# Optimization experiments

Measured on AMD Instinct MI355X. Metric: run time of the kernel, lower is better.

Reference implementation:

```python
import jax, jax.numpy as jnp
import numpy as np
import math

D_MODEL, N_HEADS, D_HEAD, D_MLP = 768, 12, 64, 3072
EPS = 1e-5
IGNORE = -100000.0


def _ln(x, w, b):
    mu = jnp.mean(x, axis=-1, keepdims=True)
    xc = x - mu
    scale = jnp.sqrt(jnp.mean(xc * xc, axis=-1, keepdims=True) + EPS)
    return (xc / scale) * w + b


def _gelu_new(x):
    # GPT-2 'new' gelu
    return 0.5 * x * (1.0 + jnp.tanh(jnp.sqrt(2.0 / jnp.pi) * (x + 0.044715 * x ** 3)))


def setup_inputs() -> dict:
    key = jax.random.key(0)
    ks = jax.random.split(key, 12)
    std = 0.02
    inp = {
        "resid_pre": jax.random.normal(ks[0], (8, 1024, D_MODEL), jnp.float32),
        "W_Q": jax.random.normal(ks[1], (N_HEADS, D_MODEL, D_HEAD), jnp.float32) * std,
        "b_Q": jnp.zeros((N_HEADS, D_HEAD), jnp.float32),
        "W_K": jax.random.normal(ks[2], (N_HEADS, D_MODEL, D_HEAD), jnp.float32) * std,
        "b_K": jnp.zeros((N_HEADS, D_HEAD), jnp.float32),
        "W_V": jax.random.normal(ks[3], (N_HEADS, D_MODEL, D_HEAD), jnp.float32) * std,
        "b_V": jnp.zeros((N_HEADS, D_HEAD), jnp.float32),
        "W_O": jax.random.normal(ks[4], (N_HEADS, D_HEAD, D_MODEL), jnp.float32) * std,
        "b_O": jnp.zeros((D_MODEL,), jnp.float32),
        "ln1_w": jnp.ones((D_MODEL,), jnp.float32),
        "ln1_b": jnp.zeros((D_MODEL,), jnp.float32),
        "ln2_w": jnp.ones((D_MODEL,), jnp.float32),
        "ln2_b": jnp.zeros((D_MODEL,), jnp.float32),
        "W_in": jax.random.normal(ks[5], (D_MODEL, D_MLP), jnp.float32) * std,
        "b_in": jnp.zeros((D_MLP,), jnp.float32),
        "W_out": jax.random.normal(ks[6], (D_MLP, D_MODEL), jnp.float32) * std,
        "b_out": jnp.zeros((D_MODEL,), jnp.float32),
    }
    return inp


def reference(resid_pre, W_Q, b_Q, W_K, b_K, W_V, b_V, W_O, b_O,
              ln1_w, ln1_b, ln2_w, ln2_b, W_in, b_in, W_out, b_out):
    # ---- ln1 + attention ----
    n = _ln(resid_pre, ln1_w, ln1_b)  # [b, s, d]; broadcast over heads in einsums
    q = jnp.einsum('bsd,hde->bshe', n, W_Q) + b_Q
    k = jnp.einsum('bsd,hde->bshe', n, W_K) + b_K
    v = jnp.einsum('bsd,hde->bshe', n, W_V) + b_V
    scores = jnp.einsum('bqhe,bkhe->bhqk', q, k) / math.sqrt(D_HEAD)
    S = scores.shape[-1]
    causal = jnp.triu(jnp.ones((S, S), dtype=bool), k=1)
    scores = jnp.where(causal, IGNORE, scores)
    pattern = jax.nn.softmax(scores, axis=-1)
    z = jnp.einsum('bhqk,bkhe->bqhe', pattern, v)
    # per-head output with b_O / n_heads each (as in source), then summed over heads
    attn_per_head = jnp.einsum('bqhe,hed->bqhd', z, W_O) + b_O / N_HEADS
    attn_out = attn_per_head.sum(axis=2)  # [b, s, d]
    resid_mid = resid_pre + attn_out
    # ---- ln2 + mlp ----
    n2 = _ln(resid_mid, ln2_w, ln2_b)
    pre = jnp.einsum('bsd,dm->bsm', n2, W_in) + b_in
    post = _gelu_new(pre)
    mlp_out = jnp.einsum('bsm,md->bsd', post, W_out) + b_out
    return resid_mid + mlp_out
```

## Files before the change

kernel.cpp:

```cpp
#include <hip/hip_runtime.h>
#include <hip/hip_bf16.h>

typedef unsigned short u16;
typedef float f32x4 __attribute__((ext_vector_type(4)));
typedef __bf16 bf16x8 __attribute__((ext_vector_type(8)));
typedef unsigned short u16x8 __attribute__((ext_vector_type(8)));
typedef unsigned short u16x4 __attribute__((ext_vector_type(4)));

__device__ __forceinline__ float b2f(u16 u) {
    unsigned v = ((unsigned)u) << 16;
    return __builtin_bit_cast(float, v);
}
__device__ __forceinline__ u16 f2b(float f) {
    unsigned u = __builtin_bit_cast(unsigned, f);
    u += 0x7fffu + ((u >> 16) & 1u);
    return (u16)(u >> 16);
}
__device__ __forceinline__ bf16x8 ldfrag(const u16* p) {
    return __builtin_bit_cast(bf16x8, *(const u16x8*)p);
}
__device__ __forceinline__ f32x4 mfma16(bf16x8 a, bf16x8 b, f32x4 c) {
    return __builtin_amdgcn_mfma_f32_16x16x32_bf16(a, b, c, 0, 0, 0);
}
__device__ __forceinline__ void gload_lds16(const u16* g, u16* l) {
    __builtin_amdgcn_global_load_lds(
        (const __attribute__((address_space(1))) unsigned int*)(g),
        (__attribute__((address_space(3))) unsigned int*)(l), 16, 0, 0);
}

#define T_TOK 8192
#define DM 768
#define NH 12
#define DH 64
#define DMLP 3072
#define SEQ 1024
#define QKV_LD 2304
#define QK_LD 1536

#define OFF_WQKV ((size_t)0)
#define OFF_WO   (OFF_WQKV + (size_t)2304*768)
#define OFF_WIN  (OFF_WO   + (size_t)768*768)
#define OFF_WOUT (OFF_WIN  + (size_t)768*3072)
#define OFF_BQKV (OFF_WOUT + (size_t)3072*768)
#define P0       (OFF_BQKV + (size_t)4608)

#define SZ_N    ((size_t)T_TOK*DM)
#define SZ_QKV  ((size_t)T_TOK*QKV_LD)
#define A_NBUF   (P0)
#define A_QKV    (P0 + SZ_N)
#define A_Z      (P0 + SZ_N + SZ_QKV)
#define A_N2     (P0)
#define A_POST   (P0 + SZ_N)
#define PATHA_BYTES (((size_t)(P0 + SZ_N + SZ_QKV + SZ_N)) * 2)
#define B_Z      (P0)
#define B_QKVB   (P0 + SZ_N)
#define B_NBUF   (B_QKVB + (size_t)SEQ*QKV_LD)
#define B_N2     (P0)
#define B_POSTC  (P0 + SZ_N)

#define TT_QKV  432
#define TT_WO   (TT_QKV + 144)
#define TT_WIN  (TT_WO + 576)
#define TT_WOUT (TT_WIN + 576)

__global__ __launch_bounds__(256) void prep_kernel(
    const float* __restrict__ WQ, const float* __restrict__ WK, const float* __restrict__ WV,
    const float* __restrict__ WO, const float* __restrict__ Win, const float* __restrict__ Wout,
    const float* __restrict__ bQ, const float* __restrict__ bK, const float* __restrict__ bV,
    u16* __restrict__ Wqkv_t, u16* __restrict__ Wo_t, u16* __restrict__ Win_t,
    u16* __restrict__ Wout_t, float* __restrict__ bias_qkv)
{
    const int bid = blockIdx.x;
    const int tid = threadIdx.x;
    if (bid == TT_WOUT) {
        for (int j = tid; j < 2304; j += 256)
            bias_qkv[j] = (j < 768) ? bQ[j] : ((j < 1536) ? bK[j - 768] : bV[j - 1536]);
        return;
    }
    __shared__ u16 tile[64][72];

    const float* sp; u16* dp;
    int sldc, dldc;
    if (bid < TT_QKV) {
        int wh = bid / 12, td = bid % 12;
        int which = wh / 12, h = wh % 12;
        const float* W = (which == 0) ? WQ : ((which == 1) ? WK : WV);
        sp = W + (size_t)h * 49152 + (size_t)(td * 64) * 64;   sldc = 64;
        dp = Wqkv_t + (size_t)(which * 768 + h * 64) * 768 + td * 64; dldc = 768;
    } else if (bid < TT_WO) {
        int t2 = bid - TT_QKV, ti = t2 / 12, tj = t2 % 12;
        sp = WO + (size_t)(ti * 64) * 768 + tj * 64;           sldc = 768;
        dp = Wo_t + (size_t)(tj * 64) * 768 + ti * 64;         dldc = 768;
    } else if (bid < TT_WIN) {
        int t3 = bid - TT_WO, ti = t3 / 48, tj = t3 % 48;
        sp = Win + (size_t)(ti * 64) * 3072 + tj * 64;         sldc = 3072;
        dp = Win_t + (size_t)(tj * 64) * 768 + ti * 64;        dldc = 768;
    } else {
        int t4 = bid - TT_WIN, ti = t4 / 12, tj = t4 % 12;
        sp = Wout + (size_t)(ti * 64) * 768 + tj * 64;         sldc = 768;
        dp = Wout_t + (size_t)(tj * 64) * 3072 + ti * 64;      dldc = 3072;
    }

    {
        int r = tid >> 2, cseg = (tid & 3) * 16;
        const float* src = sp + (size_t)r * sldc + cseg;
#pragma unroll
        for (int j = 0; j < 16; j++)
            tile[cseg + j][r] = f2b(src[j]);
    }
    __syncthreads();
    {
        int r2 = tid >> 2, c2seg = (tid & 3) * 16;
        u16* dst = dp + (size_t)r2 * dldc + c2seg;
        *(u16x8*)dst       = *(const u16x8*)&tile[r2][c2seg];
        *(u16x8*)(dst + 8) = *(const u16x8*)&tile[r2][c2seg + 8];
    }
}

__global__ __launch_bounds__(256) void ln_kernel(
    const float* __restrict__ x, const float* __restrict__ w,
    const float* __restrict__ bb, u16* __restrict__ out)
{
    __shared__ float red[4];
    size_t base = (size_t)blockIdx.x * DM;
    int tid = threadIdx.x;
    float v0 = x[base + tid], v1 = x[base + tid + 256], v2 = x[base + tid + 512];
    float s = v0 + v1 + v2;
#pragma unroll
    for (int off = 32; off > 0; off >>= 1) s += __shfl_xor(s, off);
    if ((tid & 63) == 0) red[tid >> 6] = s;
    __syncthreads();
    float mu = (red[0] + red[1] + red[2] + red[3]) * (1.0f / 768.0f);
    v0 -= mu; v1 -= mu; v2 -= mu;
    float q = v0 * v0 + v1 * v1 + v2 * v2;
    __syncthreads();
#pragma unroll
    for (int off = 32; off > 0; off >>= 1) q += __shfl_xor(q, off);
    if ((tid & 63) == 0) red[tid >> 6] = q;
    __syncthreads();
    float var = (red[0] + red[1] + red[2] + red[3]) * (1.0f / 768.0f);
    float sc = rsqrtf(var + 1e-5f);
    out[base + tid]       = f2b(v0 * sc * w[tid]       + bb[tid]);
    out[base + tid + 256] = f2b(v1 * sc * w[tid + 256] + bb[tid + 256]);
    out[base + tid + 512] = f2b(v2 * sc * w[tid + 512] + bb[tid + 512]);
}

template <int EPI, int TM>
__global__ __launch_bounds__(256) void gemm_bt_kernel(
    const u16* __restrict__ A, const u16* __restrict__ BT,
    const float* __restrict__ bias, const float* __restrict__ aux,
    void* __restrict__ outp, int N, int K)
{
    __shared__ __align__(16) u16 As[3][TM * 32];
    __shared__ __align__(16) u16 Bs[3][128 * 32];
    const int tid = threadIdx.x;
    const int w = tid >> 6, l = tid & 63;
    const int lr = l & 15, lq = l >> 4;
    const int bm = blockIdx.x * TM, bn = blockIdx.y * 128;
    constexpr int MT = TM / 32;
    constexpr bool TR = (EPI != 4);
    const int wm = (w >> 1) * (TM / 2), wn = (w & 1) * 64;

    f32x4 acc[MT][4];
#pragma unroll
    for (int i = 0; i < MT; i++)
#pragma unroll
        for (int j = 0; j < 4; j++) acc[i][j] = f32x4{0.f, 0.f, 0.f, 0.f};

    const int srow_a = (TM == 128) ? (w * 32 + (l >> 2)) : (w * 16 + (l >> 2));
    const int srow_b = w * 32 + (l >> 2);
    const int scol = (l & 3) * 8;
    const u16* Ab = A  + (size_t)(bm + srow_a) * K + scol;
    const u16* Bb = BT + (size_t)(bn + srow_b) * K + scol;
    const int asd = (TM == 128) ? w * 1024 : w * 512;
    const int bsd = w * 1024;

    const int kiter = K >> 5;

#define STAGE_T(kk, s)                                                      \
    {   const int k0_ = (kk) * 32;                                          \
        gload_lds16(Ab + k0_, &As[s][asd]);                                 \
        if constexpr (TM == 128) gload_lds16(Ab + 16 * K + k0_, &As[s][asd + 512]); \
        gload_lds16(Bb + k0_,          &Bs[s][bsd]);                        \
        gload_lds16(Bb + 16 * K + k0_, &Bs[s][bsd + 512]);  }

    STAGE_T(0, 0);
    STAGE_T(1, 1);

    int cur = 0;
    for (int t = 0; t < kiter; ++t) {
        if (t + 1 < kiter) {
            if constexpr (TM == 128) asm volatile("s_waitcnt vmcnt(4)" ::: "memory");
            else                     asm volatile("s_waitcnt vmcnt(3)" ::: "memory");
        } else {
            asm volatile("s_waitcnt vmcnt(0)" ::: "memory");
        }
        __builtin_amdgcn_s_barrier();
        __builtin_amdgcn_sched_barrier(0);

        const u16* Asc = &As[cur][0];
        const u16* Bsc = &Bs[cur][0];
        bf16x8 af[MT], bf[4];
#pragma unroll
        for (int mt = 0; mt < MT; mt++) af[mt] = ldfrag(&Asc[(wm + mt * 16 + lr) * 32 + lq * 8]);
#pragma unroll
        for (int nt = 0; nt < 4; nt++) bf[nt] = ldfrag(&Bsc[(wn + nt * 16 + lr) * 32 + lq * 8]);
#pragma unroll
        for (int mt = 0; mt < MT; mt++)
#pragma unroll
            for (int nt = 0; nt < 4; nt++)
                acc[mt][nt] = TR ? mfma16(bf[nt], af[mt], acc[mt][nt])
                                 : mfma16(af[mt], bf[nt], acc[mt][nt]);

        if (t + 2 < kiter) {
            int nb = cur + 2; if (nb >= 3) nb -= 3;
            STAGE_T(t + 2, nb);
        }
        cur = (cur + 1 == 3) ? 0 : cur + 1;
    }
#undef STAGE_T

    if (EPI == 4) {
        const bool isv = (bn >= 1536);
        u16* vtg = (u16*)aux;
#pragma unroll
        for (int mt = 0; mt < MT; mt++) {
            int row0 = bm + wm + mt * 16 + lq * 4;
            if (!isv) {
#pragma unroll
                for (int r = 0; r < 4; r++) {
                    size_t ro = (size_t)(row0 + r) * QK_LD;
#pragma unroll
                    for (int nt = 0; nt < 4; nt++) {
                        int col = bn + wn + nt * 16 + lr;
                        ((u16*)outp)[ro + col] = f2b(acc[mt][nt][r] + bias[col]);
                    }
                }
            } else {
                int bloc = row0 >> 10;
                int s = row0 & 1023;
#pragma unroll
                for (int nt = 0; nt < 4; nt++) {
                    int col = bn + wn + nt * 16 + lr;
                    int he = col - 1536;
                    float bcol = bias[col];
                    u16x4 pk;
                    pk[0] = f2b(acc[mt][nt][0] + bcol);
                    pk[1] = f2b(acc[mt][nt][1] + bcol);
                    pk[2] = f2b(acc[mt][nt][2] + bcol);
                    pk[3] = f2b(acc[mt][nt][3] + bcol);
                    *(u16x4*)&vtg[(size_t)bloc * (NH * 64 * SEQ)
                                  + (size_t)he * SEQ + s] = pk;
                }
            }
        }
        return;
    }

#pragma unroll
    for (int mt = 0; mt < MT; mt++) {
        int row = bm + wm + mt * 16 + lr;
        size_t ro = (size_t)row * N;
#pragma unroll
        for (int nt = 0; nt < 4; nt++) {
            int col0 = bn + wn + nt * 16 + lq * 4;
            f32x4 v = acc[mt][nt] + *(const f32x4*)&bias[col0];
            if (EPI == 0) {
                u16x4 pk;
#pragma unroll
                for (int r = 0; r < 4; r++) pk[r] = f2b(v[r]);
                *(u16x4*)&((u16*)outp)[ro + col0] = pk;
            } else if (EPI == 2) {
                u16x4 pk;
#pragma unroll
                for (int r = 0; r < 4; r++) {
                    float x = v[r];
                    float y = 0.7978845608028654f * (x + 0.044715f * x * x * x);
                    pk[r] = f2b(x / (1.0f + __expf(-2.0f * y)));
                }
                *(u16x4*)&((u16*)outp)[ro + col0] = pk;
            } else {
                f32x4 a4 = *(const f32x4*)&aux[ro + col0];
                v += a4;
                *(f32x4*)&((float*)outp)[ro + col0] = v;
            }
        }
    }
}

__global__ __launch_bounds__(256, 4) void attn_kernel(
    const u16* __restrict__ qk, const u16* __restrict__ vtg,
    u16* __restrict__ z, int b0, int bq0)
{
    __shared__ __align__(16) u16 Ks[64 * 72];
    __shared__ __align__(16) u16 Vt[64 * 72];
    __shared__ __align__(16) u16 Ps[4][16 * 72];

    const int qt = (int)(gridDim.x - 1) - (int)blockIdx.x;
    const int bh = blockIdx.y;
    const int b = b0 + bh / NH, h = bh % NH;
    const int tid = threadIdx.x, w = tid >> 6, l = tid & 63;
    const int lr = l & 15, lq = l >> 4;
    const int qbase = qt * 128;
    const u16* qp = qk + (size_t)(b - bq0) * SEQ * QK_LD + h * 64;
    const u16* kp = qp + 768;
    const u16* vthead = vtg + ((size_t)(b - bq0) * NH + h) * (64 * SEQ);
    u16* PsW = &Ps[w][0];

    bf16x8 aq[2][2];
#pragma unroll
    for (int g = 0; g < 2; g++) {
        const u16* qrow = qp + (size_t)(qbase + w * 32 + g * 16 + lr) * QK_LD + lq * 8;
        aq[g][0] = ldfrag(qrow);
        aq[g][1] = ldfrag(qrow + 32);
    }

    float m_i[2] = {-1e30f, -1e30f};
    float l_i[2] = {0.f, 0.f};
    f32x4 O[2][4];
#pragma unroll
    for (int g = 0; g < 2; g++)
#pragma unroll
        for (int i = 0; i < 4; i++) O[g][i] = f32x4{0.f, 0.f, 0.f, 0.f};

    const int nkt = 2 * qt + 2;
    const int srow = tid >> 2;
    const int spart = (tid & 3) * 16;

    u16x8 kreg0, kreg1, vreg0, vreg1;
    {
        const u16* ks = kp + (size_t)srow * QK_LD + spart;
        kreg0 = *(const u16x8*)ks;
        kreg1 = *(const u16x8*)(ks + 8);
        const u16* vs = vthead + (size_t)srow * SEQ + spart;
        vreg0 = *(const u16x8*)vs;
        vreg1 = *(const u16x8*)(vs + 8);
    }

    for (int kt = 0; kt < nkt; ++kt) {
        __syncthreads();
        *(u16x8*)&Ks[srow * 72 + spart]     = kreg0;
        *(u16x8*)&Ks[srow * 72 + spart + 8] = kreg1;
        *(u16x8*)&Vt[srow * 72 + spart]     = vreg0;
        *(u16x8*)&Vt[srow * 72 + spart + 8] = vreg1;
        __syncthreads();
        if (kt + 1 < nkt) {
            const u16* ks = kp + (size_t)((kt + 1) * 64 + srow) * QK_LD + spart;
            kreg0 = *(const u16x8*)ks;
            kreg1 = *(const u16x8*)(ks + 8);
            const u16* vs = vthead + (size_t)srow * SEQ + (kt + 1) * 64 + spart;
            vreg0 = *(const u16x8*)vs;
            vreg1 = *(const u16x8*)(vs + 8);
        }

        const int krel = kt * 64 - qbase;

#pragma unroll
        for (int g = 0; g < 2; g++) {
            const int gq0 = w * 32 + g * 16;
            if (krel >= gq0 + 16) continue;

            f32x4 S[4];
#pragma unroll
            for (int nt = 0; nt < 4; nt++) S[nt] = f32x4{0.f, 0.f, 0.f, 0.f};
#pragma unroll
            for (int nt = 0; nt < 4; nt++) {
                bf16x8 bk0 = ldfrag(&Ks[(nt * 16 + lr) * 72 + lq * 8]);
                bf16x8 bk1 = ldfrag(&Ks[(nt * 16 + lr) * 72 + 32 + lq * 8]);
                S[nt] = mfma16(bk0, aq[g][0], S[nt]);
                S[nt] = mfma16(bk1, aq[g][1], S[nt]);
            }

            const bool diag = (krel + 63 > gq0);
            float mx = -1e30f;
#pragma unroll
            for (int nt = 0; nt < 4; nt++)
#pragma unroll
                for (int r = 0; r < 4; r++) {
                    float sv = S[nt][r] * 0.125f;
                    if (diag) sv = (krel + nt * 16 + lq * 4 + r <= gq0 + lr) ? sv : -1e30f;
                    S[nt][r] = sv;
                    mx = fmaxf(mx, sv);
                }
            mx = fmaxf(mx, __shfl_xor(mx, 16));
            mx = fmaxf(mx, __shfl_xor(mx, 32));
            float mn = fmaxf(m_i[g], mx);
            float alpha = __expf(m_i[g] - mn);
            m_i[g] = mn;
            float rs = 0.f;
#pragma unroll
            for (int nt = 0; nt < 4; nt++) {
                u16x4 pk;
#pragma unroll
                for (int r = 0; r < 4; r++) {
                    float pe = __expf(S[nt][r] - mn);
                    rs += pe;
                    pk[r] = f2b(pe);
                }
                *(u16x4*)&PsW[lr * 72 + nt * 16 + lq * 4] = pk;
            }
            rs += __shfl_xor(rs, 16);
            rs += __shfl_xor(rs, 32);
            l_i[g] = l_i[g] * alpha + rs;

#pragma unroll
            for (int r = 0; r < 4; r++) {
                float ar = __shfl(alpha, (l & 48) | (lq * 4 + r));
                O[g][0][r] *= ar; O[g][1][r] *= ar; O[g][2][r] *= ar; O[g][3][r] *= ar;
            }

#pragma unroll
            for (int kq = 0; kq < 2; kq++) {
                bf16x8 ap = ldfrag(&PsW[lr * 72 + kq * 32 + lq * 8]);
#pragma unroll
                for (int ot = 0; ot < 4; ot++) {
                    bf16x8 bv = ldfrag(&Vt[(ot * 16 + lr) * 72 + kq * 32 + lq * 8]);
                    O[g][ot] = mfma16(ap, bv, O[g][ot]);
                }
            }
        }
    }

#pragma unroll
    for (int g = 0; g < 2; g++) {
        float li[4];
#pragma unroll
        for (int r = 0; r < 4; r++)
            li[r] = __shfl(l_i[g], (l & 48) | (lq * 4 + r));
#pragma unroll
        for (int ot = 0; ot < 4; ot++)
#pragma unroll
            for (int r = 0; r < 4; r++) {
                int q = qbase + w * 32 + g * 16 + lq * 4 + r;
                size_t t = (size_t)b * SEQ + q;
                z[t * DM + h * 64 + ot * 16 + lr] = f2b(O[g][ot][r] / li[r]);
            }
    }
}

extern "C" void kernel_launch(void* const* d_in, const int* in_sizes, int n_in,
                              void* d_out, int out_size, void* d_ws, size_t ws_size,
                              hipStream_t stream) {
    const float* resid_pre = (const float*)d_in[0];
    const float* W_Q  = (const float*)d_in[1];
    const float* b_Q  = (const float*)d_in[2];
    const float* W_K  = (const float*)d_in[3];
    const float* b_K  = (const float*)d_in[4];
    const float* W_V  = (const float*)d_in[5];
    const float* b_V  = (const float*)d_in[6];
    const float* W_O  = (const float*)d_in[7];
    const float* b_O  = (const float*)d_in[8];
    const float* ln1w = (const float*)d_in[9];
    const float* ln1b = (const float*)d_in[10];
    const float* ln2w = (const float*)d_in[11];
    const float* ln2b = (const float*)d_in[12];
    const float* W_in  = (const float*)d_in[13];
    const float* b_in  = (const float*)d_in[14];
    const float* W_out = (const float*)d_in[15];
    const float* b_out = (const float*)d_in[16];

    u16* ws16       = (u16*)d_ws;
    u16* Wqkv_t     = ws16 + OFF_WQKV;
    u16* Wo_t       = ws16 + OFF_WO;
    u16* Win_t      = ws16 + OFF_WIN;
    u16* Wout_t     = ws16 + OFF_WOUT;
    float* bias_qkv = (float*)(ws16 + OFF_BQKV);
    float* outp  = (float*)d_out;
    float* resid = (float*)d_out;

    prep_kernel<<<TT_WOUT + 1, 256, 0, stream>>>(
        W_Q, W_K, W_V, W_O, W_in, W_out, b_Q, b_K, b_V,
        Wqkv_t, Wo_t, Win_t, Wout_t, bias_qkv);

    if (ws_size >= PATHA_BYTES) {
        u16* nbuf    = ws16 + A_NBUF;
        u16* qkbuf   = ws16 + A_QKV;
        u16* vtgA    = ws16 + A_QKV + (size_t)T_TOK * QK_LD;
        u16* zbuf    = ws16 + A_Z;
        u16* n2buf   = ws16 + A_N2;
        u16* postbuf = ws16 + A_POST;

        ln_kernel<<<T_TOK, 256, 0, stream>>>(resid_pre, ln1w, ln1b, nbuf);
        gemm_bt_kernel<4, 128><<<dim3(T_TOK / 128, QKV_LD / 128), 256, 0, stream>>>(
            nbuf, Wqkv_t, bias_qkv, (const float*)vtgA, qkbuf, QKV_LD, DM);
        attn_kernel<<<dim3(SEQ / 128, 8 * NH), 256, 0, stream>>>(qkbuf, vtgA, zbuf, 0, 0);
        gemm_bt_kernel<1, 64><<<dim3(T_TOK / 64, DM / 128), 256, 0, stream>>>(
            zbuf, Wo_t, b_O, resid_pre, resid, DM, DM);
        ln_kernel<<<T_TOK, 256, 0, stream>>>(resid, ln2w, ln2b, n2buf);
        gemm_bt_kernel<2, 128><<<dim3(T_TOK / 128, DMLP / 128), 256, 0, stream>>>(
            n2buf, Win_t, b_in, nullptr, postbuf, DMLP, DM);
        gemm_bt_kernel<3, 64><<<dim3(T_TOK / 64, DM / 128), 256, 0, stream>>>(
            postbuf, Wout_t, b_out, resid, outp, DM, DMLP);
    } else {
        u16* zbuf   = ws16 + B_Z;
        u16* qkb    = ws16 + B_QKVB;
        u16* vtgB   = qkb + (size_t)SEQ * QK_LD;
        u16* nbuf   = ws16 + B_NBUF;
        u16* n2buf  = ws16 + B_N2;
        u16* postc  = ws16 + B_POSTC;

        ln_kernel<<<T_TOK, 256, 0, stream>>>(resid_pre, ln1w, ln1b, nbuf);
        for (int b = 0; b < 8; b++) {
            gemm_bt_kernel<4, 128><<<dim3(SEQ / 128, QKV_LD / 128), 256, 0, stream>>>(
                nbuf + (size_t)b * SEQ * DM, Wqkv_t, bias_qkv, (const float*)vtgB, qkb, QKV_LD, DM);
            attn_kernel<<<dim3(SEQ / 128, NH), 256, 0, stream>>>(qkb, vtgB, zbuf, b, b);
        }
        gemm_bt_kernel<1, 64><<<dim3(T_TOK / 64, DM / 128), 256, 0, stream>>>(
            zbuf, Wo_t, b_O, resid_pre, resid, DM, DM);
        ln_kernel<<<T_TOK, 256, 0, stream>>>(resid, ln2w, ln2b, n2buf);
        for (int c = 0; c < 4; c++) {
            const size_t r0 = (size_t)c * 2048;
            gemm_bt_kernel<2, 128><<<dim3(2048 / 128, DMLP / 128), 256, 0, stream>>>(
                n2buf + r0 * DM, Win_t, b_in, nullptr, postc, DMLP, DM);
            gemm_bt_kernel<3, 64><<<dim3(2048 / 64, DM / 128), 256, 0, stream>>>(
                postc, Wout_t, b_out, resid + r0 * DM, outp + r0 * DM, DM, DMLP);
        }
    }
}
```

Baseline: 413.5 us.

## Shrink attention query tile to 64 rows, one 16-row group per wave

The attention kernel now processes 64 query rows per block instead of 128, so each wave handles a single 16-row group and the grid doubles along the sequence axis. The causal mask is simplified to apply only on the diagonal key tile, and the launch bound is raised to allow five blocks per CU. This aims for more parallelism and better load balance across the causal triangle, with fewer registers per thread. The cost is that K/V tiles are reloaded from global memory by twice as many blocks.

```diff
diff --git a/kernel.cpp b/kernel.cpp
--- a/kernel.cpp
+++ b/kernel.cpp
@@ -288,7 +288,7 @@
     }
 }
 
-__global__ __launch_bounds__(256, 4) void attn_kernel(
+__global__ __launch_bounds__(256, 5) void attn_kernel(
     const u16* __restrict__ qk, const u16* __restrict__ vtg,
     u16* __restrict__ z, int b0, int bq0)
 {
@@ -301,29 +301,26 @@
     const int b = b0 + bh / NH, h = bh % NH;
     const int tid = threadIdx.x, w = tid >> 6, l = tid & 63;
     const int lr = l & 15, lq = l >> 4;
-    const int qbase = qt * 128;
+    const int qbase = qt * 64;
     const u16* qp = qk + (size_t)(b - bq0) * SEQ * QK_LD + h * 64;
     const u16* kp = qp + 768;
     const u16* vthead = vtg + ((size_t)(b - bq0) * NH + h) * (64 * SEQ);
     u16* PsW = &Ps[w][0];
 
-    bf16x8 aq[2][2];
-#pragma unroll
-    for (int g = 0; g < 2; g++) {
-        const u16* qrow = qp + (size_t)(qbase + w * 32 + g * 16 + lr) * QK_LD + lq * 8;
-        aq[g][0] = ldfrag(qrow);
-        aq[g][1] = ldfrag(qrow + 32);
-    }
-
-    float m_i[2] = {-1e30f, -1e30f};
-    float l_i[2] = {0.f, 0.f};
-    f32x4 O[2][4];
-#pragma unroll
-    for (int g = 0; g < 2; g++)
-#pragma unroll
-        for (int i = 0; i < 4; i++) O[g][i] = f32x4{0.f, 0.f, 0.f, 0.f};
-
-    const int nkt = 2 * qt + 2;
+    bf16x8 aq0, aq1;
+    {
+        const u16* qrow = qp + (size_t)(qbase + w * 16 + lr) * QK_LD + lq * 8;
+        aq0 = ldfrag(qrow);
+        aq1 = ldfrag(qrow + 32);
+    }
+
+    float m_i = -1e30f;
+    float l_i = 0.f;
+    f32x4 O[4];
+#pragma unroll
+    for (int i = 0; i < 4; i++) O[i] = f32x4{0.f, 0.f, 0.f, 0.f};
+
+    const int nkt = qt + 1;
     const int srow = tid >> 2;
     const int spart = (tid & 3) * 16;
 
@@ -353,89 +350,78 @@
             vreg1 = *(const u16x8*)(vs + 8);
         }
 
-        const int krel = kt * 64 - qbase;
-
-#pragma unroll
-        for (int g = 0; g < 2; g++) {
-            const int gq0 = w * 32 + g * 16;
-            if (krel >= gq0 + 16) continue;
-
-            f32x4 S[4];
-#pragma unroll
-            for (int nt = 0; nt < 4; nt++) S[nt] = f32x4{0.f, 0.f, 0.f, 0.f};
-#pragma unroll
-            for (int nt = 0; nt < 4; nt++) {
-                bf16x8 bk0 = ldfrag(&Ks[(nt * 16 + lr) * 72 + lq * 8]);
-                bf16x8 bk1 = ldfrag(&Ks[(nt * 16 + lr) * 72 + 32 + lq * 8]);
-                S[nt] = mfma16(bk0, aq[g][0], S[nt]);
-                S[nt] = mfma16(bk1, aq[g][1], S[nt]);
+        f32x4 S[4];
+#pragma unroll
+        for (int nt = 0; nt < 4; nt++) S[nt] = f32x4{0.f, 0.f, 0.f, 0.f};
+#pragma unroll
+        for (int nt = 0; nt < 4; nt++) {
+            bf16x8 bk0 = ldfrag(&Ks[(nt * 16 + lr) * 72 + lq * 8]);
+            bf16x8 bk1 = ldfrag(&Ks[(nt * 16 + lr) * 72 + 32 + lq * 8]);
+            S[nt] = mfma16(bk0, aq0, S[nt]);
+            S[nt] = mfma16(bk1, aq1, S[nt]);
+        }
+
+        const bool diag = (kt == qt);
+        float mx = -1e30f;
+#pragma unroll
+        for (int nt = 0; nt < 4; nt++)
+#pragma unroll
+            for (int r = 0; r < 4; r++) {
+                float sv = S[nt][r] * 0.125f;
+                if (diag) sv = (nt * 16 + lq * 4 + r <= w * 16 + lr) ? sv : -1e30f;
+                S[nt][r] = sv;
+                mx = fmaxf(mx, sv);
             }
-
-            const bool diag = (krel + 63 > gq0);
-            float mx = -1e30f;
-#pragma unroll
-            for (int nt = 0; nt < 4; nt++)
-#pragma unroll
-                for (int r = 0; r < 4; r++) {
-                    float sv = S[nt][r] * 0.125f;
-                    if (diag) sv = (krel + nt * 16 + lq * 4 + r <= gq0 + lr) ? sv : -1e30f;
-                    S[nt][r] = sv;
-                    mx = fmaxf(mx, sv);
-                }
-            mx = fmaxf(mx, __shfl_xor(mx, 16));
-            mx = fmaxf(mx, __shfl_xor(mx, 32));
-            float mn = fmaxf(m_i[g], mx);
-            float alpha = __expf(m_i[g] - mn);
-            m_i[g] = mn;
-            float rs = 0.f;
-#pragma unroll
-            for (int nt = 0; nt < 4; nt++) {
-                u16x4 pk;
-#pragma unroll
-                for (int r = 0; r < 4; r++) {
-                    float pe = __expf(S[nt][r] - mn);
-                    rs += pe;
-                    pk[r] = f2b(pe);
-                }
-                *(u16x4*)&PsW[lr * 72 + nt * 16 + lq * 4] = pk;
+        mx = fmaxf(mx, __shfl_xor(mx, 16));
+        mx = fmaxf(mx, __shfl_xor(mx, 32));
+        float mn = fmaxf(m_i, mx);
+        float alpha = __expf(m_i - mn);
+        m_i = mn;
+        float rs = 0.f;
+#pragma unroll
+        for (int nt = 0; nt < 4; nt++) {
+            u16x4 pk;
+#pragma unroll
+            for (int r = 0; r < 4; r++) {
+                float pe = __expf(S[nt][r] - mn);
+                rs += pe;
+                pk[r] = f2b(pe);
             }
-            rs += __shfl_xor(rs, 16);
-            rs += __shfl_xor(rs, 32);
-            l_i[g] = l_i[g] * alpha + rs;
-
-#pragma unroll
-            for (int r = 0; r < 4; r++) {
-                float ar = __shfl(alpha, (l & 48) | (lq * 4 + r));
-                O[g][0][r] *= ar; O[g][1][r] *= ar; O[g][2][r] *= ar; O[g][3][r] *= ar;
+            *(u16x4*)&PsW[lr * 72 + nt * 16 + lq * 4] = pk;
+        }
+        rs += __shfl_xor(rs, 16);
+        rs += __shfl_xor(rs, 32);
+        l_i = l_i * alpha + rs;
+
+#pragma unroll
+        for (int r = 0; r < 4; r++) {
+            float ar = __shfl(alpha, (l & 48) | (lq * 4 + r));
+            O[0][r] *= ar; O[1][r] *= ar; O[2][r] *= ar; O[3][r] *= ar;
+        }
+
+#pragma unroll
+        for (int kq = 0; kq < 2; kq++) {
+            bf16x8 ap = ldfrag(&PsW[lr * 72 + kq * 32 + lq * 8]);
+#pragma unroll
+            for (int ot = 0; ot < 4; ot++) {
+                bf16x8 bv = ldfrag(&Vt[(ot * 16 + lr) * 72 + kq * 32 + lq * 8]);
+                O[ot] = mfma16(ap, bv, O[ot]);
             }
-
-#pragma unroll
-            for (int kq = 0; kq < 2; kq++) {
-                bf16x8 ap = ldfrag(&PsW[lr * 72 + kq * 32 + lq * 8]);
-#pragma unroll
-                for (int ot = 0; ot < 4; ot++) {
-                    bf16x8 bv = ldfrag(&Vt[(ot * 16 + lr) * 72 + kq * 32 + lq * 8]);
-                    O[g][ot] = mfma16(ap, bv, O[g][ot]);
-                }
-            }
-        }
-    }
-
-#pragma unroll
-    for (int g = 0; g < 2; g++) {
-        float li[4];
-#pragma unroll
-        for (int r = 0; r < 4; r++)
-            li[r] = __shfl(l_i[g], (l & 48) | (lq * 4 + r));
-#pragma unroll
-        for (int ot = 0; ot < 4; ot++)
-#pragma unroll
-            for (int r = 0; r < 4; r++) {
-                int q = qbase + w * 32 + g * 16 + lq * 4 + r;
-                size_t t = (size_t)b * SEQ + q;
-                z[t * DM + h * 64 + ot * 16 + lr] = f2b(O[g][ot][r] / li[r]);
-            }
-    }
+        }
+    }
+
+    float li[4];
+#pragma unroll
+    for (int r = 0; r < 4; r++)
+        li[r] = __shfl(l_i, (l & 48) | (lq * 4 + r));
+#pragma unroll
+    for (int ot = 0; ot < 4; ot++)
+#pragma unroll
+        for (int r = 0; r < 4; r++) {
+            int q = qbase + w * 16 + lq * 4 + r;
+            size_t t = (size_t)b * SEQ + q;
+            z[t * DM + h * 64 + ot * 16 + lr] = f2b(O[ot][r] / li[r]);
+        }
 }
 
 extern "C" void kernel_launch(void* const* d_in, const int* in_sizes, int n_in,
@@ -483,7 +469,7 @@
         ln_kernel<<<T_TOK, 256, 0, stream>>>(resid_pre, ln1w, ln1b, nbuf);
         gemm_bt_kernel<4, 128><<<dim3(T_TOK / 128, QKV_LD / 128), 256, 0, stream>>>(
             nbuf, Wqkv_t, bias_qkv, (const float*)vtgA, qkbuf, QKV_LD, DM);
-        attn_kernel<<<dim3(SEQ / 128, 8 * NH), 256, 0, stream>>>(qkbuf, vtgA, zbuf, 0, 0);
+        attn_kernel<<<dim3(SEQ / 64, 8 * NH), 256, 0, stream>>>(qkbuf, vtgA, zbuf, 0, 0);
         gemm_bt_kernel<1, 64><<<dim3(T_TOK / 64, DM / 128), 256, 0, stream>>>(
             zbuf, Wo_t, b_O, resid_pre, resid, DM, DM);
         ln_kernel<<<T_TOK, 256, 0, stream>>>(resid, ln2w, ln2b, n2buf);
@@ -503,7 +489,7 @@
         for (int b = 0; b < 8; b++) {
             gemm_bt_kernel<4, 128><<<dim3(SEQ / 128, QKV_LD / 128), 256, 0, stream>>>(
                 nbuf + (size_t)b * SEQ * DM, Wqkv_t, bias_qkv, (const float*)vtgB, qkb, QKV_LD, DM);
-            attn_kernel<<<dim3(SEQ / 128, NH), 256, 0, stream>>>(qkb, vtgB, zbuf, b, b);
+            attn_kernel<<<dim3(SEQ / 64, NH), 256, 0, stream>>>(qkb, vtgB, zbuf, b, b);
         }
         gemm_bt_kernel<1, 64><<<dim3(T_TOK / 64, DM / 128), 256, 0, stream>>>(
             zbuf, Wo_t, b_O, resid_pre, resid, DM, DM);
```

Result: faster. 395.8 us (-4.3%).
